# Optimization experiments

Measured on AMD Instinct MI355X. Metric: run time of the kernel, lower is better.

Reference implementation:

```python
import jax, jax.numpy as jnp
import numpy as np

B, T, I, H = 4096, 128, 32, 64


def _u(key, shape, bound):
    return jax.random.uniform(key, shape, jnp.float32, -bound, bound)


def setup_inputs() -> dict:
    key = jax.random.key(0)
    ks = jax.random.split(key, 14)
    bound = 1.0 / np.sqrt(H)  # torch LSTM/Linear default init scale
    inp = {
        "x": jax.random.normal(ks[0], (B, T, I), jnp.float32),
        "Wih0": _u(ks[1], (4 * H, I), bound),
        "Whh0": _u(ks[2], (4 * H, H), bound),
        "bih0": _u(ks[3], (4 * H,), bound),
        "bhh0": _u(ks[4], (4 * H,), bound),
        "Wih1": _u(ks[5], (4 * H, H), bound),
        "Whh1": _u(ks[6], (4 * H, H), bound),
        "bih1": _u(ks[7], (4 * H,), bound),
        "bhh1": _u(ks[8], (4 * H,), bound),
        "Wc1": _u(ks[9], (32, H), 1.0 / np.sqrt(H)),
        "bc1": _u(ks[10], (32,), 1.0 / np.sqrt(H)),
        "Wc2": _u(ks[11], (1, 32), 1.0 / np.sqrt(32)),
        "bc2": _u(ks[12], (1,), 1.0 / np.sqrt(32)),
    }
    return inp


def lstm_layer(x_tbi, Wih, Whh, bih, bhh):
    """x_tbi: [T, B, in]. Returns (all hidden [T,B,H], final hidden [B,H]).
    PyTorch gate order: i, f, g, o."""
    b = x_tbi.shape[1]
    h0 = jnp.zeros((b, Whh.shape[1]), x_tbi.dtype)
    c0 = jnp.zeros_like(h0)
    # precompute input projections for all timesteps in one big GEMM
    xproj = jnp.einsum('tbi,gi->tbg', x_tbi, Wih) + (bih + bhh)

    def step(carry, xp_t):
        h, c = carry
        gates = xp_t + h @ Whh.T  # [B, 4H]
        i, f, g, o = jnp.split(gates, 4, axis=-1)
        c = jax.nn.sigmoid(f) * c + jax.nn.sigmoid(i) * jnp.tanh(g)
        h = jax.nn.sigmoid(o) * jnp.tanh(c)
        return (h, c), h

    (hT, _), hs = jax.lax.scan(step, (h0, c0), xproj)
    return hs, hT


def reference(x, Wih0, Whh0, bih0, bhh0, Wih1, Whh1, bih1, bhh1, Wc1, bc1, Wc2, bc2):
    x_tbi = jnp.transpose(x, (1, 0, 2))  # [T, B, I]
    hs0, _ = lstm_layer(x_tbi, Wih0, Whh0, bih0, bhh0)
    # dropout between layers is identity in eval mode
    _, hT = lstm_layer(hs0, Wih1, Whh1, bih1, bhh1)  # h_n[-1]: [B, H]
    hidden = jax.nn.relu(hT @ Wc1.T + bc1)  # [B, 32]; classifier dropout = identity (eval)
    out = hidden @ Wc2.T + bc2  # [B, 1]
    return out.squeeze(-1)  # [B]
```

## Files before the change

kernel.cpp:

```cpp
#include <hip/hip_runtime.h>


#define TT 128
#define II 32
#define D0 8

typedef _Float16 half8 __attribute__((ext_vector_type(8)));
typedef float floatx4 __attribute__((ext_vector_type(4)));

#define LOG2E 1.4426950408889634f

__device__ __forceinline__ half8 cvt_frag(float4 a, float4 b) {
    half8 h;
    h[0] = (_Float16)a.x; h[1] = (_Float16)a.y; h[2] = (_Float16)a.z; h[3] = (_Float16)a.w;
    h[4] = (_Float16)b.x; h[5] = (_Float16)b.y; h[6] = (_Float16)b.z; h[7] = (_Float16)b.w;
    return h;
}

__device__ __forceinline__ half8 load_w_frag(const float* __restrict__ W, int n, int K, int k0) {
    const float* p = W + (size_t)n * K + k0;
    return cvt_frag(*(const float4*)p, *(const float4*)(p + 4));
}

__device__ __forceinline__ void wait_ge(int* p, int v) {
    while (__hip_atomic_load(p, __ATOMIC_ACQUIRE, __HIP_MEMORY_SCOPE_WORKGROUP) < v)
        __builtin_amdgcn_s_sleep(1);
}

__device__ __forceinline__ void lstm_cell(const floatx4* a, float* cr, float* hnew,
                                          float nbi, float nbf, float bg2, float nbo) {
    const float nL  = -LOG2E;
    const float p2L = 2.0f * LOG2E;
    const float C43 = 30.0f * LOG2E;
    #pragma unroll
    for (int r = 0; r < 4; ++r) {
        float vf = __builtin_amdgcn_exp2f(fmaf(a[1][r], nL, nbf));
        float sf = __builtin_amdgcn_rcpf(1.0f + vf);
        float tg = __builtin_amdgcn_fmed3f(fmaf(a[2][r], p2L, bg2), -C43, C43);
        float u  = __builtin_amdgcn_exp2f(tg);
        float vi = __builtin_amdgcn_exp2f(fmaf(a[0][r], nL, nbi));
        float d1 = u + 1.0f;
        float st = (u - 1.0f) * __builtin_amdgcn_rcpf(fmaf(vi, d1, d1));
        float c  = fmaf(sf, cr[r], st);
        cr[r] = c;
        float vo = __builtin_amdgcn_exp2f(fmaf(a[3][r], nL, nbo));
        float tc = __builtin_amdgcn_fmed3f(c * p2L, -C43, C43);
        float uc = __builtin_amdgcn_exp2f(tc);
        float dc = uc + 1.0f;
        hnew[r] = (uc - 1.0f) * __builtin_amdgcn_rcpf(fmaf(vo, dc, dc));
    }
}

__global__ __launch_bounds__(512, 2) void lstm_fused(
    const float* __restrict__ x,
    const float* __restrict__ Wih0, const float* __restrict__ Whh0,
    const float* __restrict__ bih0, const float* __restrict__ bhh0,
    const float* __restrict__ Wih1, const float* __restrict__ Whh1,
    const float* __restrict__ bih1, const float* __restrict__ bhh1,
    const float* __restrict__ Wc1, const float* __restrict__ bc1,
    const float* __restrict__ Wc2, const float* __restrict__ bc2,
    float* __restrict__ out)
{
    __shared__ __align__(16) _Float16 xs[2][16][40];
    __shared__ __align__(16) _Float16 h0s[D0][16][72];
    __shared__ __align__(16) _Float16 h1s[2][16][72];
    __shared__ __align__(16) float h1f[16][68];
    __shared__ float hid[16][32];
    __shared__ int c0[TT + 1];
    __shared__ int c1[TT + 1];

    const int tid  = threadIdx.x;
    const int wid  = tid >> 6;
    const int w4   = wid & 3;
    const bool isL0 = (wid < 4);
    const int lane = tid & 63;
    const int q  = lane >> 4;
    const int lr = lane & 15;
    const int b0 = blockIdx.x * 16;

    const float nL  = -LOG2E;
    const float p2L = 2.0f * LOG2E;

    half8 bx0[4], bh0[4][2];
    half8 bi1[4][2], bh1[4][2];
    float bias[4];
    if (isL0) {
        #pragma unroll
        for (int g = 0; g < 4; ++g) {
            int n = (w4 + 4 * g) * 16 + lr;
            bx0[g]    = load_w_frag(Wih0, n, 32, q * 8);
            bh0[g][0] = load_w_frag(Whh0, n, 64, q * 8);
            bh0[g][1] = load_w_frag(Whh0, n, 64, 32 + q * 8);
            bias[g]   = bih0[n] + bhh0[n];
        }
    } else {
        #pragma unroll
        for (int g = 0; g < 4; ++g) {
            int n = (w4 + 4 * g) * 16 + lr;
            bi1[g][0] = load_w_frag(Wih1, n, 64, q * 8);
            bi1[g][1] = load_w_frag(Wih1, n, 64, 32 + q * 8);
            bh1[g][0] = load_w_frag(Whh1, n, 64, q * 8);
            bh1[g][1] = load_w_frag(Whh1, n, 64, 32 + q * 8);
            bias[g]   = bih1[n] + bhh1[n];
        }
    }
    const float nbi = nL * bias[0], nbf = nL * bias[1];
    const float bg2 = p2L * bias[2], nbo = nL * bias[3];
    const floatx4 zeroq = {0.f, 0.f, 0.f, 0.f};

    for (int i = tid; i < 16 * 72; i += 512) {
        ((_Float16*)h0s[D0 - 1])[i] = (_Float16)0.0f;
        ((_Float16*)h1s[1])[i]      = (_Float16)0.0f;
    }
    for (int i = tid; i <= TT; i += 512) { c0[i] = 0; c1[i] = 0; }

    const int xm = (tid >> 4) & 15;
    const int xf = (tid & 15) * 2;
    const float* xrow = x + ((size_t)(b0 + xm) * TT) * II + xf;
    float2 xbuf = {0.f, 0.f};
    if (isL0) {
        float2 x0 = *(const float2*)(xrow);
        xs[0][xm][xf]     = (_Float16)x0.x;
        xs[0][xm][xf + 1] = (_Float16)x0.y;
        xbuf = *(const float2*)(xrow + II);
    }
    __syncthreads();

    float cr[4] = {0.f, 0.f, 0.f, 0.f};
    float hnew[4];
    floatx4 a[4];

    if (isL0) {
        for (int t = 0; t < TT; ++t) {
            if (t > 0)   wait_ge(&c0[t - 1], 4);
            if (t >= D0) wait_ge(&c1[t - D0], 4);
            const int rs = (t + D0 - 1) & (D0 - 1);
            half8 xfrag = *(const half8*)&xs[t & 1][lr][q * 8];
            half8 h0a   = *(const half8*)&h0s[rs][lr][q * 8];
            half8 h0b   = *(const half8*)&h0s[rs][lr][32 + q * 8];
            float2 xnew = xbuf;
            if (t + 2 < TT) xnew = *(const float2*)(xrow + (size_t)(t + 2) * II);
            #pragma unroll
            for (int g = 0; g < 4; ++g) {
                floatx4 acc = __builtin_amdgcn_mfma_f32_16x16x32_f16(xfrag, bx0[g],    zeroq, 0, 0, 0);
                acc         = __builtin_amdgcn_mfma_f32_16x16x32_f16(h0a,   bh0[g][0], acc,   0, 0, 0);
                a[g]        = __builtin_amdgcn_mfma_f32_16x16x32_f16(h0b,   bh0[g][1], acc,   0, 0, 0);
            }
            lstm_cell(a, cr, hnew, nbi, nbf, bg2, nbo);
            #pragma unroll
            for (int r = 0; r < 4; ++r)
                h0s[t & (D0 - 1)][q * 4 + r][w4 * 16 + lr] = (_Float16)hnew[r];
            if (t + 1 < TT) {
                xs[(t + 1) & 1][xm][xf]     = (_Float16)xbuf.x;
                xs[(t + 1) & 1][xm][xf + 1] = (_Float16)xbuf.y;
            }
            xbuf = xnew;
            if (lane == 0)
                __hip_atomic_fetch_add(&c0[t], 1, __ATOMIC_RELEASE, __HIP_MEMORY_SCOPE_WORKGROUP);
        }
    } else {
        for (int t = 0; t < TT; ++t) {
            wait_ge(&c0[t], 4);
            if (t > 0) wait_ge(&c1[t - 1], 4);
            const int hs = t & (D0 - 1);
            const int ps = (t + 1) & 1;
            half8 g0a = *(const half8*)&h0s[hs][lr][q * 8];
            half8 g0b = *(const half8*)&h0s[hs][lr][32 + q * 8];
            half8 h1a = *(const half8*)&h1s[ps][lr][q * 8];
            half8 h1b = *(const half8*)&h1s[ps][lr][32 + q * 8];
            #pragma unroll
            for (int g = 0; g < 4; ++g) {
                floatx4 acc = __builtin_amdgcn_mfma_f32_16x16x32_f16(g0a, bi1[g][0], zeroq, 0, 0, 0);
                acc         = __builtin_amdgcn_mfma_f32_16x16x32_f16(g0b, bi1[g][1], acc,   0, 0, 0);
                acc         = __builtin_amdgcn_mfma_f32_16x16x32_f16(h1a, bh1[g][0], acc,   0, 0, 0);
                a[g]        = __builtin_amdgcn_mfma_f32_16x16x32_f16(h1b, bh1[g][1], acc,   0, 0, 0);
            }
            lstm_cell(a, cr, hnew, nbi, nbf, bg2, nbo);
            if (t == TT - 1) {
                #pragma unroll
                for (int r = 0; r < 4; ++r)
                    h1f[q * 4 + r][w4 * 16 + lr] = hnew[r];
            } else {
                #pragma unroll
                for (int r = 0; r < 4; ++r)
                    h1s[t & 1][q * 4 + r][w4 * 16 + lr] = (_Float16)hnew[r];
            }
            if (lane == 0)
                __hip_atomic_fetch_add(&c1[t], 1, __ATOMIC_RELEASE, __HIP_MEMORY_SCOPE_WORKGROUP);
        }
    }
    __syncthreads();

    if (tid < 256) {
        int m = tid >> 4;
        int u = (tid & 15) * 2;
        float aa = bc1[u], bb = bc1[u + 1];
        const float* w0 = Wc1 + u * 64;
        const float* w1 = Wc1 + (u + 1) * 64;
        #pragma unroll 8
        for (int kk = 0; kk < 64; ++kk) {
            float hv = h1f[m][kk];
            aa += hv * w0[kk];
            bb += hv * w1[kk];
        }
        hid[m][u]     = fmaxf(aa, 0.f);
        hid[m][u + 1] = fmaxf(bb, 0.f);
    }
    __syncthreads();
    if (tid < 16) {
        float o = bc2[0];
        #pragma unroll
        for (int u = 0; u < 32; ++u) o += hid[tid][u] * Wc2[u];
        out[b0 + tid] = o;
    }
}

extern "C" void kernel_launch(void* const* d_in, const int* in_sizes, int n_in,
                              void* d_out, int out_size, void* d_ws, size_t ws_size,
                              hipStream_t stream) {
    (void)in_sizes; (void)n_in; (void)d_ws; (void)ws_size; (void)out_size;
    const float* x    = (const float*)d_in[0];
    const float* Wih0 = (const float*)d_in[1];
    const float* Whh0 = (const float*)d_in[2];
    const float* bih0 = (const float*)d_in[3];
    const float* bhh0 = (const float*)d_in[4];
    const float* Wih1 = (const float*)d_in[5];
    const float* Whh1 = (const float*)d_in[6];
    const float* bih1 = (const float*)d_in[7];
    const float* bhh1 = (const float*)d_in[8];
    const float* Wc1  = (const float*)d_in[9];
    const float* bc1  = (const float*)d_in[10];
    const float* Wc2  = (const float*)d_in[11];
    const float* bc2  = (const float*)d_in[12];
    lstm_fused<<<dim3(256), dim3(512), 0, stream>>>(
        x, Wih0, Whh0, bih0, bhh0, Wih1, Whh1, bih1, bhh1, Wc1, bc1, Wc2, bc2,
        (float*)d_out);
}
```

Before: 217.0 us.

## Replace atomic flag handoff with barrier-phased software pipeline and batched reciprocals

Replaces the per-step shared-memory atomic counters and spin-waits between layer-0 and layer-1 waves with a lockstep schedule of two __syncthreads per step. Layer-0 MFMA overlaps layer-1 cell math in one phase, and layer-0 cell math overlaps layer-1 MFMA in the other. The h0 ring buffer shrinks from 8 slots to 2. The LSTM cell also batches reciprocals by multiplying denominators pairwise, cutting rcp count. This drops spin-wait and atomic latency but forces strict lockstep with block-wide barriers, and the combined denominators could overflow or underflow for extreme values.

```diff
diff --git a/kernel.cpp b/kernel.cpp
--- a/kernel.cpp
+++ b/kernel.cpp
@@ -3,7 +3,6 @@
 
 #define TT 128
 #define II 32
-#define D0 8
 
 typedef _Float16 half8 __attribute__((ext_vector_type(8)));
 typedef float floatx4 __attribute__((ext_vector_type(4)));
@@ -22,33 +21,50 @@
     return cvt_frag(*(const float4*)p, *(const float4*)(p + 4));
 }
 
-__device__ __forceinline__ void wait_ge(int* p, int v) {
-    while (__hip_atomic_load(p, __ATOMIC_ACQUIRE, __HIP_MEMORY_SCOPE_WORKGROUP) < v)
-        __builtin_amdgcn_s_sleep(1);
-}
-
-__device__ __forceinline__ void lstm_cell(const floatx4* a, float* cr, float* hnew,
-                                          float nbi, float nbf, float bg2, float nbo) {
+__device__ __forceinline__ void lstm_cell4(const floatx4* a, float* cr, float* hnew,
+                                           float nbi, float nbf, float bg2, float nbo) {
     const float nL  = -LOG2E;
     const float p2L = 2.0f * LOG2E;
     const float C43 = 30.0f * LOG2E;
+    float m[4], numc[4];
     #pragma unroll
     for (int r = 0; r < 4; ++r) {
         float vf = __builtin_amdgcn_exp2f(fmaf(a[1][r], nL, nbf));
-        float sf = __builtin_amdgcn_rcpf(1.0f + vf);
         float tg = __builtin_amdgcn_fmed3f(fmaf(a[2][r], p2L, bg2), -C43, C43);
         float u  = __builtin_amdgcn_exp2f(tg);
         float vi = __builtin_amdgcn_exp2f(fmaf(a[0][r], nL, nbi));
-        float d1 = u + 1.0f;
-        float st = (u - 1.0f) * __builtin_amdgcn_rcpf(fmaf(vi, d1, d1));
-        float c  = fmaf(sf, cr[r], st);
-        cr[r] = c;
+        float du = u + 1.0f;
+        float ds = fmaf(vi, du, du);
+        float df = 1.0f + vf;
+        m[r]    = df * ds;
+        numc[r] = fmaf(cr[r], ds, (u - 1.0f) * df);
+    }
+    float p01 = m[0] * m[1], p23 = m[2] * m[3];
+    float r01 = __builtin_amdgcn_rcpf(p01);
+    float r23 = __builtin_amdgcn_rcpf(p23);
+    float c0 = numc[0] * (r01 * m[1]);
+    float c1 = numc[1] * (r01 * m[0]);
+    float c2 = numc[2] * (r23 * m[3]);
+    float c3 = numc[3] * (r23 * m[2]);
+    float c[4] = {c0, c1, c2, c3};
+    float dh[4], un[4];
+    #pragma unroll
+    for (int r = 0; r < 4; ++r) {
+        cr[r] = c[r];
         float vo = __builtin_amdgcn_exp2f(fmaf(a[3][r], nL, nbo));
-        float tc = __builtin_amdgcn_fmed3f(c * p2L, -C43, C43);
+        float tc = __builtin_amdgcn_fmed3f(c[r] * p2L, -C43, C43);
         float uc = __builtin_amdgcn_exp2f(tc);
-        float dc = uc + 1.0f;
-        hnew[r] = (uc - 1.0f) * __builtin_amdgcn_rcpf(fmaf(vo, dc, dc));
-    }
+        float du2 = uc + 1.0f;
+        dh[r] = fmaf(vo, du2, du2);
+        un[r] = uc - 1.0f;
+    }
+    float q01 = dh[0] * dh[1], q23 = dh[2] * dh[3];
+    float s01 = __builtin_amdgcn_rcpf(q01);
+    float s23 = __builtin_amdgcn_rcpf(q23);
+    hnew[0] = un[0] * (s01 * dh[1]);
+    hnew[1] = un[1] * (s01 * dh[0]);
+    hnew[2] = un[2] * (s23 * dh[3]);
+    hnew[3] = un[3] * (s23 * dh[2]);
 }
 
 __global__ __launch_bounds__(512, 2) void lstm_fused(
@@ -62,12 +78,10 @@
     float* __restrict__ out)
 {
     __shared__ __align__(16) _Float16 xs[2][16][40];
-    __shared__ __align__(16) _Float16 h0s[D0][16][72];
+    __shared__ __align__(16) _Float16 h0s[2][16][72];
     __shared__ __align__(16) _Float16 h1s[2][16][72];
     __shared__ __align__(16) float h1f[16][68];
     __shared__ float hid[16][32];
-    __shared__ int c0[TT + 1];
-    __shared__ int c1[TT + 1];
 
     const int tid  = threadIdx.x;
     const int wid  = tid >> 6;
@@ -108,11 +122,10 @@
     const float bg2 = p2L * bias[2], nbo = nL * bias[3];
     const floatx4 zeroq = {0.f, 0.f, 0.f, 0.f};
 
-    for (int i = tid; i < 16 * 72; i += 512) {
-        ((_Float16*)h0s[D0 - 1])[i] = (_Float16)0.0f;
-        ((_Float16*)h1s[1])[i]      = (_Float16)0.0f;
-    }
-    for (int i = tid; i <= TT; i += 512) { c0[i] = 0; c1[i] = 0; }
+    for (int i = tid; i < 2 * 16 * 72; i += 512) {
+        ((_Float16*)h0s)[i] = (_Float16)0.0f;
+        ((_Float16*)h1s)[i] = (_Float16)0.0f;
+    }
 
     const int xm = (tid >> 4) & 15;
     const int xf = (tid & 15) * 2;
@@ -124,69 +137,65 @@
         xs[0][xm][xf + 1] = (_Float16)x0.y;
         xbuf = *(const float2*)(xrow + II);
     }
-    __syncthreads();
 
     float cr[4] = {0.f, 0.f, 0.f, 0.f};
     float hnew[4];
-    floatx4 a[4];
-
-    if (isL0) {
-        for (int t = 0; t < TT; ++t) {
-            if (t > 0)   wait_ge(&c0[t - 1], 4);
-            if (t >= D0) wait_ge(&c1[t - D0], 4);
-            const int rs = (t + D0 - 1) & (D0 - 1);
-            half8 xfrag = *(const half8*)&xs[t & 1][lr][q * 8];
-            half8 h0a   = *(const half8*)&h0s[rs][lr][q * 8];
-            half8 h0b   = *(const half8*)&h0s[rs][lr][32 + q * 8];
-            float2 xnew = xbuf;
-            if (t + 2 < TT) xnew = *(const float2*)(xrow + (size_t)(t + 2) * II);
+    floatx4 a0[4];
+    floatx4 a1[4];
+
+    for (int k = 0; k < TT + 2; ++k) {
+        __syncthreads();
+        const bool l0k = isL0 && (k < TT);
+        float2 xnew = xbuf;
+        if (l0k) {
+            half8 xfrag = *(const half8*)&xs[k & 1][lr][q * 8];
+            half8 h0a   = *(const half8*)&h0s[(k + 1) & 1][lr][q * 8];
+            half8 h0b   = *(const half8*)&h0s[(k + 1) & 1][lr][32 + q * 8];
+            if (k + 2 < TT) xnew = *(const float2*)(xrow + (size_t)(k + 2) * II);
             #pragma unroll
             for (int g = 0; g < 4; ++g) {
                 floatx4 acc = __builtin_amdgcn_mfma_f32_16x16x32_f16(xfrag, bx0[g],    zeroq, 0, 0, 0);
                 acc         = __builtin_amdgcn_mfma_f32_16x16x32_f16(h0a,   bh0[g][0], acc,   0, 0, 0);
-                a[g]        = __builtin_amdgcn_mfma_f32_16x16x32_f16(h0b,   bh0[g][1], acc,   0, 0, 0);
-            }
-            lstm_cell(a, cr, hnew, nbi, nbf, bg2, nbo);
-            #pragma unroll
-            for (int r = 0; r < 4; ++r)
-                h0s[t & (D0 - 1)][q * 4 + r][w4 * 16 + lr] = (_Float16)hnew[r];
-            if (t + 1 < TT) {
-                xs[(t + 1) & 1][xm][xf]     = (_Float16)xbuf.x;
-                xs[(t + 1) & 1][xm][xf + 1] = (_Float16)xbuf.y;
-            }
-            xbuf = xnew;
-            if (lane == 0)
-                __hip_atomic_fetch_add(&c0[t], 1, __ATOMIC_RELEASE, __HIP_MEMORY_SCOPE_WORKGROUP);
-        }
-    } else {
-        for (int t = 0; t < TT; ++t) {
-            wait_ge(&c0[t], 4);
-            if (t > 0) wait_ge(&c1[t - 1], 4);
-            const int hs = t & (D0 - 1);
-            const int ps = (t + 1) & 1;
-            half8 g0a = *(const half8*)&h0s[hs][lr][q * 8];
-            half8 g0b = *(const half8*)&h0s[hs][lr][32 + q * 8];
-            half8 h1a = *(const half8*)&h1s[ps][lr][q * 8];
-            half8 h1b = *(const half8*)&h1s[ps][lr][32 + q * 8];
-            #pragma unroll
-            for (int g = 0; g < 4; ++g) {
-                floatx4 acc = __builtin_amdgcn_mfma_f32_16x16x32_f16(g0a, bi1[g][0], zeroq, 0, 0, 0);
-                acc         = __builtin_amdgcn_mfma_f32_16x16x32_f16(g0b, bi1[g][1], acc,   0, 0, 0);
-                acc         = __builtin_amdgcn_mfma_f32_16x16x32_f16(h1a, bh1[g][0], acc,   0, 0, 0);
-                a[g]        = __builtin_amdgcn_mfma_f32_16x16x32_f16(h1b, bh1[g][1], acc,   0, 0, 0);
-            }
-            lstm_cell(a, cr, hnew, nbi, nbf, bg2, nbo);
-            if (t == TT - 1) {
+                a0[g]       = __builtin_amdgcn_mfma_f32_16x16x32_f16(h0b,   bh0[g][1], acc,   0, 0, 0);
+            }
+        }
+        if (!isL0 && k >= 2) {
+            lstm_cell4(a1, cr, hnew, nbi, nbf, bg2, nbo);
+            if (k - 2 == TT - 1) {
                 #pragma unroll
                 for (int r = 0; r < 4; ++r)
                     h1f[q * 4 + r][w4 * 16 + lr] = hnew[r];
             } else {
                 #pragma unroll
                 for (int r = 0; r < 4; ++r)
-                    h1s[t & 1][q * 4 + r][w4 * 16 + lr] = (_Float16)hnew[r];
-            }
-            if (lane == 0)
-                __hip_atomic_fetch_add(&c1[t], 1, __ATOMIC_RELEASE, __HIP_MEMORY_SCOPE_WORKGROUP);
+                    h1s[k & 1][q * 4 + r][w4 * 16 + lr] = (_Float16)hnew[r];
+            }
+        }
+
+        __syncthreads();
+        if (l0k) {
+            lstm_cell4(a0, cr, hnew, nbi, nbf, bg2, nbo);
+            #pragma unroll
+            for (int r = 0; r < 4; ++r)
+                h0s[k & 1][q * 4 + r][w4 * 16 + lr] = (_Float16)hnew[r];
+            if (k + 1 < TT) {
+                xs[(k + 1) & 1][xm][xf]     = (_Float16)xbuf.x;
+                xs[(k + 1) & 1][xm][xf + 1] = (_Float16)xbuf.y;
+            }
+            xbuf = xnew;
+        }
+        if (!isL0 && k >= 1 && k <= TT) {
+            half8 g0a = *(const half8*)&h0s[(k - 1) & 1][lr][q * 8];
+            half8 g0b = *(const half8*)&h0s[(k - 1) & 1][lr][32 + q * 8];
+            half8 h1a = *(const half8*)&h1s[k & 1][lr][q * 8];
+            half8 h1b = *(const half8*)&h1s[k & 1][lr][32 + q * 8];
+            #pragma unroll
+            for (int g = 0; g < 4; ++g) {
+                floatx4 acc = __builtin_amdgcn_mfma_f32_16x16x32_f16(g0a, bi1[g][0], zeroq, 0, 0, 0);
+                acc         = __builtin_amdgcn_mfma_f32_16x16x32_f16(g0b, bi1[g][1], acc,   0, 0, 0);
+                acc         = __builtin_amdgcn_mfma_f32_16x16x32_f16(h1a, bh1[g][0], acc,   0, 0, 0);
+                a1[g]       = __builtin_amdgcn_mfma_f32_16x16x32_f16(h1b, bh1[g][1], acc,   0, 0, 0);
+            }
         }
     }
     __syncthreads();
```

New measurement: 227.9 us. +5.0%, slower.
